# Performance work log

Hardware: AMD Instinct MI355X
Metric: run time of the kernel (lower is better)

The kernel has to match this reference:

```python
import jax, jax.numpy as jnp
import numpy as np

N = 100000      # nodes
E = 1600000     # edges (avg degree 16)
D = 128         # input feature dim
UNITS = 64      # ChebyNet units
K = 3           # Chebyshev order
C = 40          # num_classes
LMAX = 2.0      # lambda_max for rw-normalized Laplacian


def setup_inputs() -> dict:
    key = jax.random.key(0)
    ks = jax.random.split(key, 6)
    x = jax.random.normal(ks[0], (N, D), dtype=jnp.float32)
    edge_index = jax.random.randint(ks[1], (2, E), 0, N, dtype=jnp.int32)
    edge_weight = jax.random.uniform(ks[2], (E,), dtype=jnp.float32)
    W = jax.random.normal(ks[3], (K, D, UNITS), dtype=jnp.float32) * 0.05   # per-order Cheb kernels
    b = jnp.zeros((UNITS,), dtype=jnp.float32)
    Wd = jax.random.normal(ks[4], (UNITS, C), dtype=jnp.float32) * 0.05     # final Dense
    bd = jnp.zeros((C,), dtype=jnp.float32)
    return {"x": x, "edge_index": edge_index, "edge_weight": edge_weight,
            "W": W, "b": b, "Wd": Wd, "bd": bd}


def reference(x, edge_index, edge_weight, W, b, Wd, bd):
    src, dst = edge_index[0], edge_index[1]
    # rw normalization: A_hat = D^{-1} A, deg computed at dst
    deg = jax.ops.segment_sum(edge_weight, dst, num_segments=N)
    w_norm = edge_weight / jnp.maximum(deg[dst], 1e-12)  # [E]

    def lhat(h):
        # L h = h - D^{-1} A h ; L_hat = (2/lmax) L - I
        ah = jax.ops.segment_sum(h[src] * w_norm[:, None], dst, num_segments=N)  # [N, D]
        return (2.0 / LMAX) * (h - ah) - h

    # Chebyshev recursion T_0 = x, T_1 = L_hat x, T_2 = 2 L_hat T_1 - T_0
    T0 = x
    T1 = lhat(T0)
    T2 = 2.0 * lhat(T1) - T0
    h = T0 @ W[0] + T1 @ W[1] + T2 @ W[2] + b  # [N, UNITS]
    return h @ Wd + bd                          # [N, C]
```

## Files before the change

### kernel.cpp

```cpp
#include <hip/hip_runtime.h>

namespace {
constexpr int N = 100000;
constexpr int E = 1600000;
constexpr int D = 128;
constexpr int U = 64;
constexpr int C = 40;
constexpr int C2 = C / 2;
constexpr int RP = 32;
constexpr int SLOTS = 64;
constexpr int NB = (N + 255) / 256;
constexpr int CAP = 4608;
constexpr int EPB = 16;
constexpr int TPB = 256;
constexpr int GK = 136;
constexpr int PROJ_BLOCKS = (N + 63) / 64;

constexpr size_t OFF_BCUR = 0;
constexpr size_t OFF_META = OFF_BCUR + 512;
constexpr size_t OFF_CSR = OFF_META + (size_t)2 * N;
constexpr size_t OFF_BBUF = OFF_CSR + (size_t)2 * N * SLOTS;
constexpr size_t BBUF_INTS = (size_t)NB * CAP * 2;
constexpr size_t OFF_P1 = OFF_BBUF + BBUF_INTS;
constexpr size_t OFF_P2B = OFF_P1 + (size_t)N * C + 32;
constexpr size_t OFF_RBF = OFF_P2B + (size_t)N * RP;
constexpr size_t OFF_GBF = OFF_RBF + (size_t)N * RP;
constexpr size_t OFF_BC = OFF_GBF + 128 * GK / 2;

constexpr int SMEM_PROJ = 64 * GK * 2 + 128 * GK * 2 + ((C * 4 + 15) & ~15);
}

__device__ inline unsigned f2bf(float x) {
    unsigned u = __float_as_uint(x);
    return (u + 0x7fffu + ((u >> 16) & 1u)) >> 16;
}
__device__ inline unsigned pack_bf2(float a, float b) { return f2bf(a) | (f2bf(b) << 16); }
__device__ inline float2 unpack_bf2(unsigned v) {
    return make_float2(__uint_as_float(v << 16), __uint_as_float(v & 0xffff0000u));
}

typedef __attribute__((ext_vector_type(8))) short bf16x8;
typedef __attribute__((ext_vector_type(4))) float f32x4;

__global__ void prep_weights(const float* __restrict__ W, const float* __restrict__ b,
                             const float* __restrict__ Wd, const float* __restrict__ bd,
                             unsigned short* __restrict__ Gbf, float* __restrict__ bc,
                             int* __restrict__ bcur) {
    if (blockIdx.x == 0) {
        for (int i = threadIdx.x; i < 512; i += 256) bcur[i] = 0;
    }
    int t = blockIdx.x * blockDim.x + threadIdx.x;
    if (t < 128 * 128) {
        int n = t >> 7, k = t & 127;
        float s = 0.f;
        if (n < 40) {
            const float* W0 = W + (size_t)k * U;
            const float* W2 = W + (size_t)2 * D * U + (size_t)k * U;
            for (int u = 0; u < U; ++u) s += (W0[u] - W2[u]) * Wd[u * C + n];
        } else if (n < 80) {
            const float* W1 = W + (size_t)D * U + (size_t)k * U;
            for (int u = 0; u < U; ++u) s -= W1[u] * Wd[u * C + (n - 40)];
        } else if (n < 120) {
            const float* W2 = W + (size_t)2 * D * U + (size_t)k * U;
            for (int u = 0; u < U; ++u) s += 2.f * W2[u] * Wd[u * C + (n - 80)];
        }
        Gbf[n * GK + k] = (unsigned short)f2bf(s);
    } else if (t < 128 * 128 + C) {
        int c = t - 128 * 128;
        float s = bd[c];
        for (int u = 0; u < U; ++u) s += b[u] * Wd[u * C + c];
        bc[c] = s;
    }
}

__global__ __launch_bounds__(TPB) void bucket_scatter(const int* __restrict__ src,
                                                      const int* __restrict__ dst,
                                                      const float* __restrict__ ew,
                                                      int* __restrict__ bcur,
                                                      int2* __restrict__ bbuf2) {
    __shared__ int hist[NB];
    __shared__ int base[NB];
    int t = threadIdx.x;
    for (int i = t; i < NB; i += TPB) hist[i] = 0;
    __syncthreads();

    size_t e0 = (size_t)blockIdx.x * (TPB * EPB);
    int ms[EPB], md[EPB], mw[EPB], mr[EPB];
#pragma unroll
    for (int k = 0; k < EPB; ++k) {
        size_t e = e0 + (size_t)k * TPB + t;
        if (e < E) {
            ms[k] = src[e];
            md[k] = dst[e];
            mw[k] = __float_as_int(ew[e]);
            mr[k] = atomicAdd(&hist[md[k] >> 8], 1);
        } else {
            md[k] = -1;
        }
    }
    __syncthreads();
    for (int i = t; i < NB; i += TPB) {
        int c = hist[i];
        base[i] = c ? atomicAdd(&bcur[i], c) : 0;
    }
    __syncthreads();
#pragma unroll
    for (int k = 0; k < EPB; ++k) {
        if (md[k] >= 0) {
            int bkt = md[k] >> 8;
            int slot = base[bkt] + mr[k];
            if (slot < CAP)
                bbuf2[(size_t)bkt * CAP + slot] =
                    make_int2(ms[k] | ((md[k] & 255) << 24), mw[k]);
        }
    }
}

__global__ __launch_bounds__(256) void csr_and_proj(
    const int* __restrict__ bcur, const int2* __restrict__ bbuf2,
    int2* __restrict__ meta, int2* __restrict__ csr,
    const float* __restrict__ X, const unsigned* __restrict__ Gu,
    const float* __restrict__ bc, float* __restrict__ out,
    float* __restrict__ P1, unsigned short* __restrict__ P2B16) {
    __shared__ __align__(16) unsigned char smem[SMEM_PROJ];
    int t = threadIdx.x;

    if (blockIdx.x < NB) {
        int* lcur = (int*)smem;
        float* lw = (float*)(smem + 1024);
        int b = blockIdx.x;
        lcur[t] = 0;
        lw[t] = 0.f;
        __syncthreads();
        int cnt = min(bcur[b], CAP);
        for (int i = t; i < cnt; i += 256) {
            int2 r = bbuf2[(size_t)b * CAP + i];
            int idx = ((unsigned)r.x) >> 24;
            int srcn = r.x & 0x00FFFFFF;
            int slot = atomicAdd(&lcur[idx], 1);
            atomicAdd(&lw[idx], __int_as_float(r.y));
            if (slot < SLOTS)
                csr[(((size_t)(b << 8) + idx) << 6) + slot] = make_int2(srcn, r.y);
        }
        __syncthreads();
        int node = (b << 8) + t;
        if (node < N) {
            int c = min(lcur[t], SLOTS);
            float rdeg = 1.f / fmaxf(lw[t], 1e-12f);
            meta[node] = make_int2(c, __float_as_int(rdeg));
            int padded = min((c + 15) & ~15, SLOTS);
            for (int s = c; s < padded; ++s)
                csr[((size_t)node << 6) + s] = make_int2(0, 0);
        }
        return;
    }

    int rb = blockIdx.x - NB;
    unsigned short* a_s = (unsigned short*)smem;
    unsigned short* g_s = (unsigned short*)(smem + 64 * GK * 2);
    float* bc_s = (float*)(smem + 64 * GK * 2 + 128 * GK * 2);

    unsigned* gsu = (unsigned*)g_s;
    for (int i = t; i < 128 * GK / 2; i += 256) gsu[i] = Gu[i];
    if (t < C) bc_s[t] = bc[t];

#pragma unroll
    for (int i = 0; i < 8; ++i) {
        int idx = i * 256 + t;
        int row = idx >> 5, kq = idx & 31;
        size_t grow = (size_t)rb * 64 + row;
        float4 v = (grow < N) ? ((const float4*)X)[grow * 32 + kq]
                              : make_float4(0.f, 0.f, 0.f, 0.f);
        unsigned* dstp = (unsigned*)(a_s + row * GK + kq * 4);
        dstp[0] = pack_bf2(v.x, v.y);
        dstp[1] = pack_bf2(v.z, v.w);
    }
    __syncthreads();

    int w = t >> 6, l = t & 63;
    int lr = l & 15, lh = l >> 4;

    bf16x8 afr[4];
#pragma unroll
    for (int ks = 0; ks < 4; ++ks)
        afr[ks] = *(const bf16x8*)(a_s + (w * 16 + lr) * GK + ks * 32 + lh * 8);

    f32x4 acc[8];
#pragma unroll
    for (int tt = 0; tt < 8; ++tt) {
        acc[tt] = (f32x4){0.f, 0.f, 0.f, 0.f};
#pragma unroll
        for (int ks = 0; ks < 4; ++ks) {
            bf16x8 bfr = *(const bf16x8*)(g_s + (tt * 16 + lr) * GK + ks * 32 + lh * 8);
            acc[tt] = __builtin_amdgcn_mfma_f32_16x16x32_bf16(afr[ks], bfr, acc[tt], 0, 0, 0);
        }
    }

#pragma unroll
    for (int tt = 0; tt < 8; ++tt) {
        int gcol = tt * 16 + lr;
#pragma unroll
        for (int r = 0; r < 4; ++r) {
            size_t grow = (size_t)rb * 64 + w * 16 + lh * 4 + r;
            if (grow >= N) continue;
            float v = acc[tt][r];
            if (gcol < 40) {
                out[grow * C + gcol] = v + bc_s[gcol];
            } else if (gcol < 80) {
                P1[grow * C + (gcol - 40)] = v;
            } else if (gcol < 120) {
                P2B16[grow * 64 + (gcol - 80)] = (unsigned short)f2bf(v);
            }
        }
    }
}

template <bool OUT_BF>
__global__ __launch_bounds__(256) void spmm40v4(const int2* __restrict__ meta,
                                                const int2* __restrict__ csr,
                                                const unsigned* __restrict__ Xg,
                                                const float* __restrict__ Add,
                                                void* __restrict__ Yv) {
    int wid = (blockIdx.x * blockDim.x + threadIdx.x) >> 6;
    if (wid >= N) return;
    int uw = __builtin_amdgcn_readfirstlane(wid);
    int2 m = meta[uw];
    int c = m.x;
    float rdeg = __int_as_float(m.y);
    const int2* __restrict__ row = csr + ((size_t)uw << 6);
    int lane = threadIdx.x & 63;
    bool hi = lane >= 32;
    unsigned voff = (unsigned)(lane & 31);

    float2 ad = make_float2(0.f, 0.f);
    if (lane < C2) ad = ((const float2*)Add)[(size_t)wid * C2 + lane];

    float2 acc = make_float2(0.f, 0.f);
    for (int j0 = 0; j0 < c; j0 += 16) {
        unsigned va[8];
        float wa[8];
#pragma unroll
        for (int k = 0; k < 8; ++k) {
            int2 a = row[j0 + k];
            int2 b = row[j0 + 8 + k];
            int col = hi ? b.x : a.x;
            wa[k] = __int_as_float(hi ? b.y : a.y);
            va[k] = Xg[((unsigned)col << 5) + voff];
        }
#pragma unroll
        for (int k = 0; k < 8; ++k) {
            float2 v = unpack_bf2(va[k]);
            acc.x = fmaf(wa[k], v.x, acc.x);
            acc.y = fmaf(wa[k], v.y, acc.y);
        }
    }
    acc.x += __shfl_xor(acc.x, 32);
    acc.y += __shfl_xor(acc.y, 32);

    if (OUT_BF) {
        if (lane < 32) {
            unsigned o = 0u;
            if (lane < C2)
                o = pack_bf2(fmaf(acc.x, rdeg, ad.x), fmaf(acc.y, rdeg, ad.y));
            ((unsigned*)Yv)[((size_t)wid << 5) + lane] = o;
        }
    } else {
        if (lane < C2) {
            ((float2*)Yv)[(size_t)wid * C2 + lane] =
                make_float2(fmaf(acc.x, rdeg, ad.x), fmaf(acc.y, rdeg, ad.y));
        }
    }
}

extern "C" void kernel_launch(void* const* d_in, const int* in_sizes, int n_in,
                              void* d_out, int out_size, void* d_ws, size_t ws_size,
                              hipStream_t stream) {
    const float* x = (const float*)d_in[0];
    const int* ei = (const int*)d_in[1];
    const float* ew = (const float*)d_in[2];
    const float* W = (const float*)d_in[3];
    const float* b = (const float*)d_in[4];
    const float* Wd = (const float*)d_in[5];
    const float* bd = (const float*)d_in[6];
    float* out = (float*)d_out;

    const int* src = ei;
    const int* dst = ei + E;

    float* ws = (float*)d_ws;
    int* bcur = (int*)(ws + OFF_BCUR);
    int2* meta = (int2*)(ws + OFF_META);
    int2* csr = (int2*)(ws + OFF_CSR);
    int2* bbuf2 = (int2*)(ws + OFF_BBUF);
    float* P1 = ws + OFF_P1;
    unsigned* P2B = (unsigned*)(ws + OFF_P2B);
    unsigned* Rbf = (unsigned*)(ws + OFF_RBF);
    unsigned short* Gbf = (unsigned short*)(ws + OFF_GBF);
    float* bc = ws + OFF_BC;

    prep_weights<<<(128 * 128 + C + 255) / 256, 256, 0, stream>>>(W, b, Wd, bd, Gbf, bc, bcur);

    bucket_scatter<<<(E + TPB * EPB - 1) / (TPB * EPB), TPB, 0, stream>>>(src, dst, ew, bcur, bbuf2);

    csr_and_proj<<<NB + PROJ_BLOCKS, 256, 0, stream>>>(bcur, bbuf2, meta, csr, x,
                                                       (const unsigned*)Gbf, bc, out, P1,
                                                       (unsigned short*)P2B);

    spmm40v4<true><<<((size_t)N * 64 + 255) / 256, 256, 0, stream>>>(meta, csr, P2B, P1, Rbf);
    spmm40v4<false><<<((size_t)N * 64 + 255) / 256, 256, 0, stream>>>(meta, csr, Rbf, out, out);
}
```

Before: 131.1 us.

## Split CSR build from projection and make projection a persistent grid-stride MFMA kernel

```diff
diff --git a/kernel.cpp b/kernel.cpp
--- a/kernel.cpp
+++ b/kernel.cpp
@@ -14,7 +14,8 @@
 constexpr int EPB = 16;
 constexpr int TPB = 256;
 constexpr int GK = 136;
-constexpr int PROJ_BLOCKS = (N + 63) / 64;
+constexpr int NT = (N + 15) / 16;
+constexpr int PROJ_GRID = 782;
 
 constexpr size_t OFF_BCUR = 0;
 constexpr size_t OFF_META = OFF_BCUR + 512;
@@ -26,8 +27,6 @@
 constexpr size_t OFF_RBF = OFF_P2B + (size_t)N * RP;
 constexpr size_t OFF_GBF = OFF_RBF + (size_t)N * RP;
 constexpr size_t OFF_BC = OFF_GBF + 128 * GK / 2;
-
-constexpr int SMEM_PROJ = 64 * GK * 2 + 128 * GK * 2 + ((C * 4 + 15) & ~15);
 }
 
 __device__ inline unsigned f2bf(float x) {
@@ -116,100 +115,101 @@
     }
 }
 
-__global__ __launch_bounds__(256) void csr_and_proj(
-    const int* __restrict__ bcur, const int2* __restrict__ bbuf2,
-    int2* __restrict__ meta, int2* __restrict__ csr,
-    const float* __restrict__ X, const unsigned* __restrict__ Gu,
-    const float* __restrict__ bc, float* __restrict__ out,
-    float* __restrict__ P1, unsigned short* __restrict__ P2B16) {
-    __shared__ __align__(16) unsigned char smem[SMEM_PROJ];
+__global__ __launch_bounds__(256) void csr_build(const int* __restrict__ bcur,
+                                                 const int2* __restrict__ bbuf2,
+                                                 int2* __restrict__ meta,
+                                                 int2* __restrict__ csr) {
+    __shared__ int lcur[256];
+    __shared__ float lw[256];
+    int b = blockIdx.x;
     int t = threadIdx.x;
-
-    if (blockIdx.x < NB) {
-        int* lcur = (int*)smem;
-        float* lw = (float*)(smem + 1024);
-        int b = blockIdx.x;
-        lcur[t] = 0;
-        lw[t] = 0.f;
-        __syncthreads();
-        int cnt = min(bcur[b], CAP);
-        for (int i = t; i < cnt; i += 256) {
-            int2 r = bbuf2[(size_t)b * CAP + i];
-            int idx = ((unsigned)r.x) >> 24;
-            int srcn = r.x & 0x00FFFFFF;
-            int slot = atomicAdd(&lcur[idx], 1);
-            atomicAdd(&lw[idx], __int_as_float(r.y));
-            if (slot < SLOTS)
-                csr[(((size_t)(b << 8) + idx) << 6) + slot] = make_int2(srcn, r.y);
-        }
-        __syncthreads();
-        int node = (b << 8) + t;
-        if (node < N) {
-            int c = min(lcur[t], SLOTS);
-            float rdeg = 1.f / fmaxf(lw[t], 1e-12f);
-            meta[node] = make_int2(c, __float_as_int(rdeg));
-            int padded = min((c + 15) & ~15, SLOTS);
-            for (int s = c; s < padded; ++s)
-                csr[((size_t)node << 6) + s] = make_int2(0, 0);
-        }
-        return;
-    }
-
-    int rb = blockIdx.x - NB;
-    unsigned short* a_s = (unsigned short*)smem;
-    unsigned short* g_s = (unsigned short*)(smem + 64 * GK * 2);
-    float* bc_s = (float*)(smem + 64 * GK * 2 + 128 * GK * 2);
-
-    unsigned* gsu = (unsigned*)g_s;
-    for (int i = t; i < 128 * GK / 2; i += 256) gsu[i] = Gu[i];
+    lcur[t] = 0;
+    lw[t] = 0.f;
+    __syncthreads();
+    int cnt = min(bcur[b], CAP);
+    for (int i = t; i < cnt; i += 256) {
+        int2 r = bbuf2[(size_t)b * CAP + i];
+        int idx = ((unsigned)r.x) >> 24;
+        int srcn = r.x & 0x00FFFFFF;
+        int slot = atomicAdd(&lcur[idx], 1);
+        atomicAdd(&lw[idx], __int_as_float(r.y));
+        if (slot < SLOTS)
+            csr[(((size_t)(b << 8) + idx) << 6) + slot] = make_int2(srcn, r.y);
+    }
+    __syncthreads();
+    int node = (b << 8) + t;
+    if (node < N) {
+        int c = min(lcur[t], SLOTS);
+        float rdeg = 1.f / fmaxf(lw[t], 1e-12f);
+        meta[node] = make_int2(c, __float_as_int(rdeg));
+        int padded = min((c + 15) & ~15, SLOTS);
+        for (int s = c; s < padded; ++s)
+            csr[((size_t)node << 6) + s] = make_int2(0, 0);
+    }
+}
+
+__global__ __launch_bounds__(256) void proj_mfma2(const float* __restrict__ X,
+                                                  const uint4* __restrict__ Gu4,
+                                                  const float* __restrict__ bc,
+                                                  float* __restrict__ out,
+                                                  float* __restrict__ P1,
+                                                  unsigned short* __restrict__ P2B16) {
+    __shared__ __align__(16) unsigned short g_s[128 * GK];
+    __shared__ float bc_s[C];
+    int t = threadIdx.x;
+
+    uint4* gs4 = (uint4*)g_s;
+    for (int i = t; i < 128 * GK / 8; i += 256) gs4[i] = Gu4[i];
     if (t < C) bc_s[t] = bc[t];
-
-#pragma unroll
-    for (int i = 0; i < 8; ++i) {
-        int idx = i * 256 + t;
-        int row = idx >> 5, kq = idx & 31;
-        size_t grow = (size_t)rb * 64 + row;
-        float4 v = (grow < N) ? ((const float4*)X)[grow * 32 + kq]
-                              : make_float4(0.f, 0.f, 0.f, 0.f);
-        unsigned* dstp = (unsigned*)(a_s + row * GK + kq * 4);
-        dstp[0] = pack_bf2(v.x, v.y);
-        dstp[1] = pack_bf2(v.z, v.w);
-    }
     __syncthreads();
 
     int w = t >> 6, l = t & 63;
     int lr = l & 15, lh = l >> 4;
 
-    bf16x8 afr[4];
-#pragma unroll
-    for (int ks = 0; ks < 4; ++ks)
-        afr[ks] = *(const bf16x8*)(a_s + (w * 16 + lr) * GK + ks * 32 + lh * 8);
-
-    f32x4 acc[8];
-#pragma unroll
-    for (int tt = 0; tt < 8; ++tt) {
-        acc[tt] = (f32x4){0.f, 0.f, 0.f, 0.f};
+    for (int tile = blockIdx.x * 4 + w; tile < NT; tile += PROJ_GRID * 4) {
+        int row0 = tile * 16;
+        int r = min(row0 + lr, N - 1);
+        const float4* xr = (const float4*)(X + (size_t)r * D);
+
+        bf16x8 afr[4];
 #pragma unroll
         for (int ks = 0; ks < 4; ++ks) {
-            bf16x8 bfr = *(const bf16x8*)(g_s + (tt * 16 + lr) * GK + ks * 32 + lh * 8);
-            acc[tt] = __builtin_amdgcn_mfma_f32_16x16x32_bf16(afr[ks], bfr, acc[tt], 0, 0, 0);
-        }
-    }
-
-#pragma unroll
-    for (int tt = 0; tt < 8; ++tt) {
-        int gcol = tt * 16 + lr;
-#pragma unroll
-        for (int r = 0; r < 4; ++r) {
-            size_t grow = (size_t)rb * 64 + w * 16 + lh * 4 + r;
-            if (grow >= N) continue;
-            float v = acc[tt][r];
-            if (gcol < 40) {
-                out[grow * C + gcol] = v + bc_s[gcol];
-            } else if (gcol < 80) {
-                P1[grow * C + (gcol - 40)] = v;
-            } else if (gcol < 120) {
-                P2B16[grow * 64 + (gcol - 80)] = (unsigned short)f2bf(v);
+            float4 v0 = xr[ks * 8 + lh * 2];
+            float4 v1 = xr[ks * 8 + lh * 2 + 1];
+            union { unsigned u[4]; bf16x8 v; } cv;
+            cv.u[0] = pack_bf2(v0.x, v0.y);
+            cv.u[1] = pack_bf2(v0.z, v0.w);
+            cv.u[2] = pack_bf2(v1.x, v1.y);
+            cv.u[3] = pack_bf2(v1.z, v1.w);
+            afr[ks] = cv.v;
+        }
+
+        f32x4 acc[8];
+#pragma unroll
+        for (int tt = 0; tt < 8; ++tt) {
+            acc[tt] = (f32x4){0.f, 0.f, 0.f, 0.f};
+#pragma unroll
+            for (int ks = 0; ks < 4; ++ks) {
+                bf16x8 bfr = *(const bf16x8*)(g_s + (tt * 16 + lr) * GK + ks * 32 + lh * 8);
+                acc[tt] = __builtin_amdgcn_mfma_f32_16x16x32_bf16(afr[ks], bfr, acc[tt], 0, 0, 0);
+            }
+        }
+
+#pragma unroll
+        for (int tt = 0; tt < 8; ++tt) {
+            int gcol = tt * 16 + lr;
+#pragma unroll
+            for (int rr = 0; rr < 4; ++rr) {
+                size_t grow = (size_t)row0 + lh * 4 + rr;
+                if (grow >= N) continue;
+                float v = acc[tt][rr];
+                if (gcol < 40) {
+                    out[grow * C + gcol] = v + bc_s[gcol];
+                } else if (gcol < 80) {
+                    P1[grow * C + (gcol - 40)] = v;
+                } else if (gcol < 120) {
+                    P2B16[grow * 64 + (gcol - 80)] = (unsigned short)f2bf(v);
+                }
             }
         }
     }
@@ -301,10 +301,10 @@
     prep_weights<<<(128 * 128 + C + 255) / 256, 256, 0, stream>>>(W, b, Wd, bd, Gbf, bc, bcur);
 
     bucket_scatter<<<(E + TPB * EPB - 1) / (TPB * EPB), TPB, 0, stream>>>(src, dst, ew, bcur, bbuf2);
-
-    csr_and_proj<<<NB + PROJ_BLOCKS, 256, 0, stream>>>(bcur, bbuf2, meta, csr, x,
-                                                       (const unsigned*)Gbf, bc, out, P1,
-                                                       (unsigned short*)P2B);
+    csr_build<<<NB, 256, 0, stream>>>(bcur, bbuf2, meta, csr);
+
+    proj_mfma2<<<PROJ_GRID, 256, 0, stream>>>(x, (const uint4*)Gbf, bc, out, P1,
+                                              (unsigned short*)P2B);
 
     spmm40v4<true><<<((size_t)N * 64 + 255) / 256, 256, 0, stream>>>(meta, csr, P2B, P1, Rbf);
     spmm40v4<false><<<((size_t)N * 64 + 255) / 256, 256, 0, stream>>>(meta, csr, Rbf, out, out);
```

Result: slower. 143.0 us (+9.1%).

## Build compact CSR with per-node offsets and store P1 in bf16

Applied to the files above, without the earlier changes.

```diff
diff --git a/kernel.cpp b/kernel.cpp
--- a/kernel.cpp
+++ b/kernel.cpp
@@ -8,21 +8,21 @@
 constexpr int C = 40;
 constexpr int C2 = C / 2;
 constexpr int RP = 32;
-constexpr int SLOTS = 64;
 constexpr int NB = (N + 255) / 256;
 constexpr int CAP = 4608;
 constexpr int EPB = 16;
 constexpr int TPB = 256;
 constexpr int GK = 136;
 constexpr int PROJ_BLOCKS = (N + 63) / 64;
+constexpr int CSRCAP = 3200000;
 
 constexpr size_t OFF_BCUR = 0;
 constexpr size_t OFF_META = OFF_BCUR + 512;
-constexpr size_t OFF_CSR = OFF_META + (size_t)2 * N;
-constexpr size_t OFF_BBUF = OFF_CSR + (size_t)2 * N * SLOTS;
+constexpr size_t OFF_CSR = OFF_META + (size_t)4 * N;
+constexpr size_t OFF_BBUF = OFF_CSR + (size_t)2 * CSRCAP;
 constexpr size_t BBUF_INTS = (size_t)NB * CAP * 2;
-constexpr size_t OFF_P1 = OFF_BBUF + BBUF_INTS;
-constexpr size_t OFF_P2B = OFF_P1 + (size_t)N * C + 32;
+constexpr size_t OFF_P1B = OFF_BBUF + BBUF_INTS;
+constexpr size_t OFF_P2B = OFF_P1B + (size_t)N * C2;
 constexpr size_t OFF_RBF = OFF_P2B + (size_t)N * RP;
 constexpr size_t OFF_GBF = OFF_RBF + (size_t)N * RP;
 constexpr size_t OFF_BC = OFF_GBF + 128 * GK / 2;
@@ -117,40 +117,66 @@
 }
 
 __global__ __launch_bounds__(256) void csr_and_proj(
-    const int* __restrict__ bcur, const int2* __restrict__ bbuf2,
-    int2* __restrict__ meta, int2* __restrict__ csr,
+    const int* __restrict__ bcur_ro, int* __restrict__ bcur,
+    const int2* __restrict__ bbuf2,
+    int4* __restrict__ meta4, int2* __restrict__ csr,
     const float* __restrict__ X, const unsigned* __restrict__ Gu,
     const float* __restrict__ bc, float* __restrict__ out,
-    float* __restrict__ P1, unsigned short* __restrict__ P2B16) {
+    unsigned short* __restrict__ P1B16, unsigned short* __restrict__ P2B16) {
     __shared__ __align__(16) unsigned char smem[SMEM_PROJ];
     int t = threadIdx.x;
 
     if (blockIdx.x < NB) {
         int* lcur = (int*)smem;
         float* lw = (float*)(smem + 1024);
+        int* lstart = (int*)(smem + 2048);
+        int* lsc = (int*)(smem + 3072);
         int b = blockIdx.x;
         lcur[t] = 0;
         lw[t] = 0.f;
         __syncthreads();
-        int cnt = min(bcur[b], CAP);
+        int cnt = min(bcur_ro[b], CAP);
+        const int2* bb = bbuf2 + (size_t)b * CAP;
         for (int i = t; i < cnt; i += 256) {
-            int2 r = bbuf2[(size_t)b * CAP + i];
+            int2 r = bb[i];
             int idx = ((unsigned)r.x) >> 24;
-            int srcn = r.x & 0x00FFFFFF;
-            int slot = atomicAdd(&lcur[idx], 1);
+            atomicAdd(&lcur[idx], 1);
             atomicAdd(&lw[idx], __int_as_float(r.y));
-            if (slot < SLOTS)
-                csr[(((size_t)(b << 8) + idx) << 6) + slot] = make_int2(srcn, r.y);
-        }
-        __syncthreads();
+        }
+        __syncthreads();
+        int myc = lcur[t];
+        int mypc = (myc + 15) & ~15;
+        int v = mypc;
+#pragma unroll
+        for (int off = 1; off < 64; off <<= 1) {
+            int u = __shfl_up(v, off);
+            if ((t & 63) >= off) v += u;
+        }
+        int w = t >> 6;
+        if ((t & 63) == 63) lsc[w] = v;
+        __syncthreads();
+        if (t == 0) {
+            int s0 = 0;
+#pragma unroll
+            for (int i = 0; i < 4; ++i) { int c4 = lsc[i]; lsc[i] = s0; s0 += c4; }
+            lsc[4] = atomicAdd(&bcur[508], s0);
+        }
+        __syncthreads();
+        int start = lsc[4] + lsc[w] + v - mypc;
+        lstart[t] = start;
         int node = (b << 8) + t;
         if (node < N) {
-            int c = min(lcur[t], SLOTS);
             float rdeg = 1.f / fmaxf(lw[t], 1e-12f);
-            meta[node] = make_int2(c, __float_as_int(rdeg));
-            int padded = min((c + 15) & ~15, SLOTS);
-            for (int s = c; s < padded; ++s)
-                csr[((size_t)node << 6) + s] = make_int2(0, 0);
+            meta4[node] = make_int4(start, myc, __float_as_int(rdeg), 0);
+            for (int s = myc; s < mypc; ++s) csr[start + s] = make_int2(0, 0);
+        }
+        lcur[t] = 0;
+        __syncthreads();
+        for (int i = t; i < cnt; i += 256) {
+            int2 r = bb[i];
+            int idx = ((unsigned)r.x) >> 24;
+            int slot = atomicAdd(&lcur[idx], 1);
+            csr[lstart[idx] + slot] = make_int2(r.x & 0x00FFFFFF, r.y);
         }
         return;
     }
@@ -207,7 +233,7 @@
             if (gcol < 40) {
                 out[grow * C + gcol] = v + bc_s[gcol];
             } else if (gcol < 80) {
-                P1[grow * C + (gcol - 40)] = v;
+                P1B16[grow * C + (gcol - 40)] = (unsigned short)f2bf(v);
             } else if (gcol < 120) {
                 P2B16[grow * 64 + (gcol - 80)] = (unsigned short)f2bf(v);
             }
@@ -215,25 +241,31 @@
     }
 }
 
-template <bool OUT_BF>
-__global__ __launch_bounds__(256) void spmm40v4(const int2* __restrict__ meta,
+template <bool PASS1>
+__global__ __launch_bounds__(256) void spmm40v5(const int4* __restrict__ meta4,
                                                 const int2* __restrict__ csr,
                                                 const unsigned* __restrict__ Xg,
-                                                const float* __restrict__ Add,
+                                                const void* __restrict__ Add,
                                                 void* __restrict__ Yv) {
     int wid = (blockIdx.x * blockDim.x + threadIdx.x) >> 6;
     if (wid >= N) return;
     int uw = __builtin_amdgcn_readfirstlane(wid);
-    int2 m = meta[uw];
-    int c = m.x;
-    float rdeg = __int_as_float(m.y);
-    const int2* __restrict__ row = csr + ((size_t)uw << 6);
+    int4 m = meta4[uw];
+    int start = m.x;
+    int c = m.y;
+    float rdeg = __int_as_float(m.z);
+    const int2* __restrict__ row = csr + start;
     int lane = threadIdx.x & 63;
     bool hi = lane >= 32;
     unsigned voff = (unsigned)(lane & 31);
 
     float2 ad = make_float2(0.f, 0.f);
-    if (lane < C2) ad = ((const float2*)Add)[(size_t)wid * C2 + lane];
+    if (lane < C2) {
+        if (PASS1)
+            ad = unpack_bf2(((const unsigned*)Add)[(size_t)wid * C2 + lane]);
+        else
+            ad = ((const float2*)Add)[(size_t)wid * C2 + lane];
+    }
 
     float2 acc = make_float2(0.f, 0.f);
     for (int j0 = 0; j0 < c; j0 += 16) {
@@ -257,7 +289,7 @@
     acc.x += __shfl_xor(acc.x, 32);
     acc.y += __shfl_xor(acc.y, 32);
 
-    if (OUT_BF) {
+    if (PASS1) {
         if (lane < 32) {
             unsigned o = 0u;
             if (lane < C2)
@@ -289,10 +321,10 @@
 
     float* ws = (float*)d_ws;
     int* bcur = (int*)(ws + OFF_BCUR);
-    int2* meta = (int2*)(ws + OFF_META);
+    int4* meta4 = (int4*)(ws + OFF_META);
     int2* csr = (int2*)(ws + OFF_CSR);
     int2* bbuf2 = (int2*)(ws + OFF_BBUF);
-    float* P1 = ws + OFF_P1;
+    unsigned* P1B = (unsigned*)(ws + OFF_P1B);
     unsigned* P2B = (unsigned*)(ws + OFF_P2B);
     unsigned* Rbf = (unsigned*)(ws + OFF_RBF);
     unsigned short* Gbf = (unsigned short*)(ws + OFF_GBF);
@@ -302,10 +334,11 @@
 
     bucket_scatter<<<(E + TPB * EPB - 1) / (TPB * EPB), TPB, 0, stream>>>(src, dst, ew, bcur, bbuf2);
 
-    csr_and_proj<<<NB + PROJ_BLOCKS, 256, 0, stream>>>(bcur, bbuf2, meta, csr, x,
-                                                       (const unsigned*)Gbf, bc, out, P1,
+    csr_and_proj<<<NB + PROJ_BLOCKS, 256, 0, stream>>>(bcur, bcur, bbuf2, meta4, csr, x,
+                                                       (const unsigned*)Gbf, bc, out,
+                                                       (unsigned short*)P1B,
                                                        (unsigned short*)P2B);
 
-    spmm40v4<true><<<((size_t)N * 64 + 255) / 256, 256, 0, stream>>>(meta, csr, P2B, P1, Rbf);
-    spmm40v4<false><<<((size_t)N * 64 + 255) / 256, 256, 0, stream>>>(meta, csr, Rbf, out, out);
-}
+    spmm40v5<true><<<((size_t)N * 64 + 255) / 256, 256, 0, stream>>>(meta4, csr, P2B, P1B, Rbf);
+    spmm40v5<false><<<((size_t)N * 64 + 255) / 256, 256, 0, stream>>>(meta4, csr, Rbf, out, out);
+}
```

New measurement: 140.8 us. +7.4%, slower.
